# Performance work log

Hardware: AMD Instinct MI355X
Metric: run time of the kernel (lower is better)

Reference implementation:

```python
import jax, jax.numpy as jnp
import numpy as np

SCALE = 2
K = 8


def setup_inputs() -> dict:
    key = jax.random.key(0)
    k1, k2, k3 = jax.random.split(key, 3)
    m, f = 8192, 512
    y_patch = jax.random.normal(k1, (m, 64), dtype=jnp.float32)
    yd_patch = jax.random.normal(k2, (m, f), dtype=jnp.float32)
    idx_k = jax.random.randint(k3, (1, m, K), 0, m, dtype=jnp.int64)
    return {"y_patch": y_patch, "yd_patch": yd_patch, "idx_k": idx_k}


def reference(y_patch, yd_patch, idx_k):
    # y_patch: (m, f_q) -- only its leading dim m is used
    # yd_patch: (m, f) database features; idx_k: (1, m, k) neighbor indices into m
    m = y_patch.shape[0]
    yd = yd_patch.reshape(m, -1)          # (m=n, f)
    f = yd.shape[1]
    k = idx_k.shape[2]
    # Gather: torch builds z of shape (1, m, f, k) with z[0,q,c,j] = yd[idx_k[0,q,j], c].
    # Equivalent direct gather without materializing the expanded (1,m,f,n) tensor:
    z = yd[idx_k[0]]                      # (m, k, f)
    # torch permute(0,3,2,1): (1, m, f, k) -> (1, k, f, m)
    z = jnp.transpose(z, (1, 2, 0))       # (k, f, m)
    # view(1, k, f//scale, scale, m) then view(1, k*(f//scale), m*scale):
    # contiguous row-major, so a single reshape is exact.
    z_sr = z.reshape(1, k * (f // SCALE), m * SCALE)
    return z_sr
```

## Files before the change

kernel.cpp:

```cpp
#include <hip/hip_runtime.h>


#define Q 256
#define C 32
#define THREADS 256

__global__ __launch_bounds__(THREADS) void gather_transpose_kernel(
    const float* __restrict__ yd, const int* __restrict__ idx,
    float* __restrict__ out, int m, int f, int k)
{
    const int qb = blockIdx.x * Q;
    const int cb = blockIdx.y * C;
    const int j  = blockIdx.z;
    const int t  = threadIdx.x;

    __shared__ int rows[Q];
    __shared__ float lds[Q][C + 1];

    rows[t] = idx[(size_t)(qb + t) * k + j];
    __syncthreads();

    for (int lid = t; lid < Q * (C / 4); lid += THREADS) {
        const int row = lid >> 3;
        const int ch  = lid & 7;
        const float4 v = *reinterpret_cast<const float4*>(
            yd + (size_t)rows[row] * f + cb + (ch << 2));
        float* d = &lds[row][ch << 2];
        d[0] = v.x; d[1] = v.y; d[2] = v.z; d[3] = v.w;
    }
    __syncthreads();

    float* p = out + (size_t)j * f * m + (size_t)cb * m + qb + t;
    #pragma unroll 8
    for (int c = 0; c < C; ++c) {
        p[(size_t)c * m] = lds[t][c];
    }
}

extern "C" void kernel_launch(void* const* d_in, const int* in_sizes, int n_in,
                              void* d_out, int out_size, void* d_ws, size_t ws_size,
                              hipStream_t stream) {
    const float* yd = (const float*)d_in[1];
    const int* idx = (const int*)d_in[2];
    float* out = (float*)d_out;

    const int m = in_sizes[0] / 64;
    const int f = in_sizes[1] / m;
    const int k = in_sizes[2] / m;

    dim3 grid(m / Q, f / C, k);
    hipLaunchKernelGGL(gather_transpose_kernel, grid, dim3(THREADS), 0,
                       stream, yd, idx, out, m, f, k);
}
```

Baseline: 162.8 us.

## Transpose in LDS on write and emit vectorized nontemporal output stores

Gathered rows are now scattered into a channel-major LDS tile, so the output phase reads float4 from LDS and writes 16-byte nontemporal stores along m, replacing per-thread scalar strided stores. The query tile shrinks from 256 to 128 rows, which doubles the block count and shrinks LDS use; launch bounds now request 4 blocks per SM. The intent is to cut the number of store instructions and avoid polluting the cache with streaming output. The trade-off is that the column-wise LDS writes on the gather side may cause bank conflicts.

Result: no change. 163.1 us (+0.2%).

```diff
diff --git a/kernel.cpp b/kernel.cpp
--- a/kernel.cpp
+++ b/kernel.cpp
@@ -1,39 +1,52 @@
 #include <hip/hip_runtime.h>
 
 
-#define Q 256
-#define C 32
+#define QT 128
+#define CT 32
+#define QPAD 132
 #define THREADS 256
 
-__global__ __launch_bounds__(THREADS) void gather_transpose_kernel(
+typedef float f32x4 __attribute__((ext_vector_type(4)));
+
+__global__ __launch_bounds__(THREADS, 4) void gather_transpose_kernel(
     const float* __restrict__ yd, const int* __restrict__ idx,
     float* __restrict__ out, int m, int f, int k)
 {
-    const int qb = blockIdx.x * Q;
-    const int cb = blockIdx.y * C;
+    const int qb = blockIdx.x * QT;
+    const int cb = blockIdx.y * CT;
     const int j  = blockIdx.z;
     const int t  = threadIdx.x;
 
-    __shared__ int rows[Q];
-    __shared__ float lds[Q][C + 1];
+    __shared__ int rows[QT];
+    __shared__ float lds[CT][QPAD];
 
-    rows[t] = idx[(size_t)(qb + t) * k + j];
+    if (t < QT) rows[t] = idx[(size_t)(qb + t) * k + j];
     __syncthreads();
 
-    for (int lid = t; lid < Q * (C / 4); lid += THREADS) {
-        const int row = lid >> 3;
-        const int ch  = lid & 7;
-        const float4 v = *reinterpret_cast<const float4*>(
+    #pragma unroll
+    for (int it = 0; it < (QT * CT / 4) / THREADS; ++it) {
+        const int gid = it * THREADS + t;
+        const int row = gid >> 3;
+        const int ch  = gid & 7;
+        const f32x4 v = *reinterpret_cast<const f32x4*>(
             yd + (size_t)rows[row] * f + cb + (ch << 2));
-        float* d = &lds[row][ch << 2];
-        d[0] = v.x; d[1] = v.y; d[2] = v.z; d[3] = v.w;
+        const int c0 = ch << 2;
+        lds[c0 + 0][row] = v.x;
+        lds[c0 + 1][row] = v.y;
+        lds[c0 + 2][row] = v.z;
+        lds[c0 + 3][row] = v.w;
     }
     __syncthreads();
 
-    float* p = out + (size_t)j * f * m + (size_t)cb * m + qb + t;
-    #pragma unroll 8
-    for (int c = 0; c < C; ++c) {
-        p[(size_t)c * m] = lds[t][c];
+    const size_t outb = (size_t)j * f * m + (size_t)cb * m + qb;
+    #pragma unroll
+    for (int it = 0; it < (QT * CT / 4) / THREADS; ++it) {
+        const int gid = it * THREADS + t;
+        const int c  = gid >> 5;
+        const int q4 = gid & 31;
+        const f32x4 v = *reinterpret_cast<const f32x4*>(&lds[c][q4 << 2]);
+        __builtin_nontemporal_store(v, reinterpret_cast<f32x4*>(
+            out + outb + (size_t)c * m + (q4 << 2)));
     }
 }
 
@@ -48,7 +61,7 @@
     const int f = in_sizes[1] / m;
     const int k = in_sizes[2] / m;
 
-    dim3 grid(m / Q, f / C, k);
+    dim3 grid(m / QT, f / CT, k);
     hipLaunchKernelGGL(gather_transpose_kernel, grid, dim3(THREADS), 0,
                        stream, yd, idx, out, m, f, k);
 }
```
